# Optimization experiments

Hardware: AMD Instinct MI355X
Metric: run time of the kernel (lower is better)

Reference implementation:

```python
import jax, jax.numpy as jnp
import numpy as np

NUM_BATCHES = 8  # number of samples (unique batch ids in coords[:,0])
EPS = 1e-10


def setup_inputs() -> dict:
    key = jax.random.key(0)
    k1, k2, k3 = jax.random.split(key, 3)
    N, D, K = 65536, 64, 8192
    z_feats = jax.random.normal(k1, (N, D), dtype=jnp.float32)
    batch_ids = jnp.sort(jax.random.randint(k2, (N,), 0, NUM_BATCHES, dtype=jnp.int64))
    codebook = jax.random.normal(k3, (K, D), dtype=jnp.float32)  # embeddings.weight ~ N(0,1)
    return {"z_feats": z_feats, "batch_ids": batch_ids, "codebook": codebook}


def reference(z_feats, batch_ids, codebook):
    # --- nearest-code assignment (torch.cdist + argmin) ---
    # squared euclidean distances; argmin over sqrt(d2) == argmin over d2
    z_sq = jnp.sum(z_feats * z_feats, axis=1, keepdims=True)        # [N,1]
    c_sq = jnp.sum(codebook * codebook, axis=1)                     # [K]
    d2 = z_sq - 2.0 * (z_feats @ codebook.T) + c_sq[None, :]        # [N,K]
    encoding_indices = jnp.argmin(d2, axis=1)                       # [N] int

    # --- gather quantized features ---
    quantized_feats = codebook[encoding_indices]                    # [N,D]

    # --- losses ---
    commitment_loss = jnp.mean((z_feats - jax.lax.stop_gradient(quantized_feats)) ** 2)
    vq_loss = jnp.mean((quantized_feats - jax.lax.stop_gradient(z_feats)) ** 2)

    # --- straight-through estimator ---
    quantized_st = z_feats + jax.lax.stop_gradient(quantized_feats - z_feats)

    # --- per-sample codebook stats (vectorized over batches) ---
    K = codebook.shape[0]
    counts = jnp.zeros((NUM_BATCHES, K), jnp.float32).at[batch_ids, encoding_indices].add(1.0)
    totals = jnp.sum(counts, axis=1, keepdims=True)                 # [B,1]
    probs = counts / jnp.maximum(totals, 1.0)
    entropy = -jnp.sum(probs * jnp.log(probs + EPS), axis=1)        # [B]
    perplexity = jnp.exp(entropy)                                   # [B]
    unique_count = jnp.sum(counts > 0, axis=1).astype(jnp.float32)  # [B]
    avg_perplexity = jnp.mean(perplexity)
    avg_entropy = jnp.mean(entropy)
    avg_unique = jnp.mean(unique_count)

    return (quantized_st, vq_loss, commitment_loss, encoding_indices,
            avg_perplexity, avg_entropy, avg_unique)
```

## Files before the change

### kernel.cpp

```cpp
#include <hip/hip_runtime.h>
#include <math.h>

#define D64 64
#define NBATCH 8
#define CBAND 2.0f
#define CHUNK 128
#define NCHUNK 64
#define KSPL 2
#define CG 32
#define NGRP 256

typedef short s16x8 __attribute__((ext_vector_type(8)));
typedef float f32x4 __attribute__((ext_vector_type(4)));

#define GLOAD16(g, l) __builtin_amdgcn_global_load_lds( \
    (const __attribute__((address_space(1))) unsigned*)(g), \
    (__attribute__((address_space(3))) unsigned*)(l), 16, 0, 0)
#define GLOAD4(g, l) __builtin_amdgcn_global_load_lds( \
    (const __attribute__((address_space(1))) unsigned*)(g), \
    (__attribute__((address_space(3))) unsigned*)(l), 4, 0, 0)

__device__ inline unsigned short f2bf(float f) {
  unsigned u = __builtin_bit_cast(unsigned, f);
  unsigned r = (u + 0x7FFFu + ((u >> 16) & 1u)) >> 16;
  return (unsigned short)r;
}
__device__ inline float bflo(unsigned u) {
  return __builtin_bit_cast(float, (u & 0xFFFFu) << 16);
}
__device__ inline float bfhi(unsigned u) {
  return __builtin_bit_cast(float, u & 0xFFFF0000u);
}
__device__ inline unsigned pack32(float s) {
  unsigned u = __builtin_bit_cast(unsigned, s);
  return (u & 0x80000000u) ? ~u : (u | 0x80000000u);
}
__device__ inline float unpack32(unsigned u) {
  unsigned b = (u & 0x80000000u) ? (u ^ 0x80000000u) : ~u;
  return __builtin_bit_cast(float, b);
}

__global__ __launch_bounds__(256) void csq_cvt_kernel(
    const float* __restrict__ cb, float* __restrict__ csq,
    float* __restrict__ csqn, short* __restrict__ cbh,
    unsigned int* __restrict__ counts, unsigned* __restrict__ pminu,
    double* __restrict__ sse_parts, int K, int Npts) {
  int t = blockIdx.x * blockDim.x + threadIdx.x;
  if (t < NBATCH * K) counts[t] = 0u;
  if (t < Npts) pminu[t] = 0xFFFFFFFFu;
  if (t < 256) sse_parts[t] = 0.0;
  int row = t >> 6, lane = t & 63;
  if (row >= K) return;
  float v = cb[(size_t)row * D64 + lane];
  cbh[(size_t)row * D64 + lane] = (short)f2bf(v);
  v *= v;
  #pragma unroll
  for (int off = 32; off; off >>= 1) v += __shfl_xor(v, off, 64);
  if (lane == 0) { csq[row] = v; csqn[row] = -0.5f * v; }
}

__global__ __launch_bounds__(256, 4) void sweep_kernel(
    const float* __restrict__ z, const short* __restrict__ cbh,
    const float* __restrict__ csqn,
    unsigned short* __restrict__ bm, unsigned* __restrict__ pminu,
    int N, int K) {
  __shared__ short lcb[2][CHUNK * D64];
  __shared__ float lcsq[2][CHUNK];

  int w = threadIdx.x >> 6;
  int l = threadIdx.x & 63;
  int lr = l & 15, lg = l >> 4;
  int base = blockIdx.x * 128 + w * 32;
  int c0g = blockIdx.y * (NCHUNK / KSPL);

  s16x8 Z[2][2];
  #pragma unroll
  for (int pt = 0; pt < 2; ++pt) {
    int row = base + pt * 16 + lr;
    #pragma unroll
    for (int kh = 0; kh < 2; ++kh) {
      const float4* zp = reinterpret_cast<const float4*>(
          z + (size_t)row * D64 + kh * 32 + lg * 8);
      float4 p0 = zp[0], p1 = zp[1];
      s16x8 t;
      t[0] = (short)f2bf(p0.x); t[1] = (short)f2bf(p0.y);
      t[2] = (short)f2bf(p0.z); t[3] = (short)f2bf(p0.w);
      t[4] = (short)f2bf(p1.x); t[5] = (short)f2bf(p1.y);
      t[6] = (short)f2bf(p1.z); t[7] = (short)f2bf(p1.w);
      Z[pt][kh] = t;
    }
  }

  int sw = (lr & 7) << 4;
  int p0off = ((lr * 128 + lg * 16) ^ sw);
  int p1off = ((lr * 128 + 64 + lg * 16) ^ sw);
  int swl = (l >> 3) << 4;

  const char* cbbytes = (const char*)cbh;
#define STAGE(chunk, b)                                                       \
  {                                                                           \
    const char* src = cbbytes + (size_t)(chunk) * (CHUNK * 128);              \
    char* dstb = (char*)lcb[b];                                               \
    _Pragma("unroll")                                                         \
    for (int j = 0; j < 4; ++j) {                                             \
      int X = (w * 4 + j) * 1024 + l * 16;                                    \
      GLOAD16(src + (X ^ swl), dstb + (w * 4 + j) * 1024);                    \
    }                                                                         \
    const char* csrc = (const char*)(csqn + (chunk) * CHUNK) + (w & 1) * 256; \
    GLOAD4(csrc + l * 4, (char*)lcsq[b] + (w & 1) * 256);                     \
  }

  float gm0 = -INFINITY, gm1 = -INFINITY;

  auto do_chunk = [&](int cg, int b) {
    const char* pb0 = (const char*)lcb[b] + p0off;
    const char* pb1 = (const char*)lcb[b] + p1off;
    float g0 = -INFINITY, g1 = -INFINITY;
    #pragma unroll
    for (int i = 0; i < 8; ++i) {
      s16x8 CA0 = *(const s16x8*)(pb0 + i * 2048);
      s16x8 CA1 = *(const s16x8*)(pb1 + i * 2048);
      float4 cn = *(const float4*)(lcsq[b] + i * 16 + lg * 4);
      #pragma unroll
      for (int pt = 0; pt < 2; ++pt) {
        f32x4 acc = {cn.x, cn.y, cn.z, cn.w};
        acc = __builtin_amdgcn_mfma_f32_16x16x32_bf16(CA0, Z[pt][0], acc, 0, 0, 0);
        acc = __builtin_amdgcn_mfma_f32_16x16x32_bf16(CA1, Z[pt][1], acc, 0, 0, 0);
        float m = fmaxf(fmaxf(acc[0], acc[1]), fmaxf(acc[2], acc[3]));
        if (pt == 0) g0 = fmaxf(g0, m); else g1 = fmaxf(g1, m);
      }
    }
    #pragma unroll
    for (int pt = 0; pt < 2; ++pt) {
      float a = pt ? g1 : g0;
      float bb = __shfl_xor(a, 16, 64);
      float cc = __shfl_xor(a, 32, 64);
      float dd = __shfl_xor(a, 48, 64);
      float gmx = fmaxf(fmaxf(a, bb), fmaxf(cc, dd));
      if (pt == 0) gm0 = fmaxf(gm0, gmx); else gm1 = fmaxf(gm1, gmx);
      if (l < 16) {
        unsigned q0 = (unsigned)f2bf(-2.0f * a) |
                      ((unsigned)f2bf(-2.0f * bb) << 16);
        unsigned q1 = (unsigned)f2bf(-2.0f * cc) |
                      ((unsigned)f2bf(-2.0f * dd) << 16);
        unsigned short* rp = bm + (size_t)(base + pt * 16 + l) * NGRP + cg * 4;
        *reinterpret_cast<uint2*>(rp) = make_uint2(q0, q1);
      }
    }
  };

  STAGE(c0g, 0);
  __syncthreads();
  for (int c = 0; c < NCHUNK / KSPL; ++c) {
    if (c + 1 < NCHUNK / KSPL) STAGE(c0g + c + 1, (c + 1) & 1);
    do_chunk(c0g + c, c & 1);
    __syncthreads();
  }
  if (l < 16) {
    atomicMin(&pminu[base + l], pack32(-2.0f * gm0));
    atomicMin(&pminu[base + 16 + l], pack32(-2.0f * gm1));
  }
#undef STAGE
}

__global__ __launch_bounds__(256) void rescore_wave_kernel(
    const float* __restrict__ z, const float* __restrict__ cb,
    const float* __restrict__ csq, const unsigned short* __restrict__ bm,
    const unsigned* __restrict__ pminu, const int* __restrict__ batch_raw,
    float* __restrict__ out_idx, float* __restrict__ outq,
    unsigned int* __restrict__ counts, double* __restrict__ sse_parts,
    int N, int K) {
  int l = threadIdx.x & 63;
  int n = blockIdx.x * 4 + (threadIdx.x >> 6);

  float thr = unpack32(pminu[n]) + CBAND;
  uint2 u = reinterpret_cast<const uint2*>(bm + (size_t)n * NGRP)[l];
  float v0 = bflo(u.x), v1 = bfhi(u.x), v2 = bflo(u.y), v3 = bfhi(u.y);
  unsigned long long m0 = __ballot(v0 <= thr);
  unsigned long long m1 = __ballot(v1 <= thr);
  unsigned long long m2 = __ballot(v2 <= thr);
  unsigned long long m3 = __ballot(v3 <= thr);

  const float4* z4 = reinterpret_cast<const float4*>(z + (size_t)n * D64);
  float4 zz0 = z4[(l & 7) * 2];
  float4 zz1 = z4[(l & 7) * 2 + 1];

  auto next_group = [&]() -> int {
    if (m0) { int t = __builtin_ctzll(m0); m0 &= m0 - 1; return t * 4 + 0; }
    if (m1) { int t = __builtin_ctzll(m1); m1 &= m1 - 1; return t * 4 + 1; }
    if (m2) { int t = __builtin_ctzll(m2); m2 &= m2 - 1; return t * 4 + 2; }
    if (m3) { int t = __builtin_ctzll(m3); m3 &= m3 - 1; return t * 4 + 3; }
    return -1;
  };

  float b1 = INFINITY, b2 = INFINITY;
  int i1 = 0x7FFFFFFF, i2 = 0x7FFFFFFF;
  bool real = (l & 7) == 0;
  int code_idx = l >> 3;
  int ioff = code_idx >> 2;
  int sub = code_idx & 3;
  const float4* cbf4 = reinterpret_cast<const float4*>(cb);

  while (m0 | m1 | m2 | m3) {
    int g = next_group();
    int cbase = (g >> 2) * 128 + (g & 3) * 4;
    const float4* gb = cbf4 + (size_t)cbase * 16;
    #pragma unroll
    for (int rr = 0; rr < 4; ++rr) {
      int i = rr * 2 + ioff;
      int rel = (i * 16 + sub) * 16 + (l & 7) * 2;
      float4 q0 = gb[rel];
      float4 q1 = gb[rel + 1];
      float p = q0.x * zz0.x;
      p = fmaf(q0.y, zz0.y, p);
      p = fmaf(q0.z, zz0.z, p);
      p = fmaf(q0.w, zz0.w, p);
      p = fmaf(q1.x, zz1.x, p);
      p = fmaf(q1.y, zz1.y, p);
      p = fmaf(q1.z, zz1.z, p);
      p = fmaf(q1.w, zz1.w, p);
      p += __shfl_xor(p, 1, 64);
      p += __shfl_xor(p, 2, 64);
      p += __shfl_xor(p, 4, 64);
      int k = cbase + i * 16 + sub;
      float s = fmaf(-2.0f, p, csq[k]);
      float sv = real ? s : INFINITY;
      int kv = real ? k : 0x7FFFFFFF;
      bool bet1 = (sv < b1) || (sv == b1 && kv < i1);
      float cs = bet1 ? b1 : sv;  int ci = bet1 ? i1 : kv;
      b1 = bet1 ? sv : b1;        i1 = bet1 ? kv : i1;
      bool bet2 = (cs < b2) || (cs == b2 && ci < i2);
      b2 = bet2 ? cs : b2;        i2 = bet2 ? ci : i2;
    }
  }
  #pragma unroll
  for (int off = 1; off < 64; off <<= 1) {
    float o1 = __shfl_xor(b1, off, 64); int j1 = __shfl_xor(i1, off, 64);
    float o2 = __shfl_xor(b2, off, 64); int j2 = __shfl_xor(i2, off, 64);
    bool t1 = (o1 < b1) || (o1 == b1 && j1 < i1);
    float cs = t1 ? b1 : o1;  int ci = t1 ? i1 : j1;
    b1 = t1 ? o1 : b1;        i1 = t1 ? j1 : i1;
    bool t2 = (cs < b2) || (cs == b2 && ci < i2);
    b2 = t2 ? cs : b2;        i2 = t2 ? ci : i2;
    bool t3 = (o2 < b2) || (o2 == b2 && j2 < i2);
    b2 = t3 ? o2 : b2;        i2 = t3 ? j2 : i2;
  }

  int final_i = i1;
  if (i2 != 0x7FFFFFFF && (b2 - b1) < 1e-3f) {
    double zd = (double)z[(size_t)n * D64 + l];
    double t0 = zd - (double)cb[(size_t)i1 * D64 + l];
    double t1 = zd - (double)cb[(size_t)i2 * D64 + l];
    double d0 = t0 * t0, d1 = t1 * t1;
    #pragma unroll
    for (int off = 1; off < 64; off <<= 1) {
      d0 += __shfl_xor(d0, off, 64);
      d1 += __shfl_xor(d1, off, 64);
    }
    if (d1 < d0 || (d1 == d0 && i2 < i1)) final_i = i2;
  }

  float zl = z[(size_t)n * D64 + l];
  float ql = cb[(size_t)final_i * D64 + l];
  float tl = ql - zl;
  outq[(size_t)n * D64 + l] = zl + tl;
  double loc = (double)tl * tl;
  #pragma unroll
  for (int off = 1; off < 64; off <<= 1) loc += __shfl_xor(loc, off, 64);
  if (l == 0) {
    out_idx[n] = (float)final_i;
    int is64 = (batch_raw[N - 1] == 0) ? 1 : 0;
    int b = is64 ? batch_raw[2 * n] : batch_raw[n];
    atomicAdd(&counts[(size_t)b * K + final_i], 1u);
    atomicAdd(&sse_parts[n & 255], loc);
  }
}

__global__ __launch_bounds__(256) void stats_kernel(
    const unsigned int* __restrict__ counts,
    double* __restrict__ perp, double* __restrict__ ent,
    double* __restrict__ uniq, int K) {
  __shared__ double sh4[4], she[4], shu[4];
  int b = blockIdx.x;
  const unsigned int* c = counts + (size_t)b * K;
  int lane = threadIdx.x & 63, w = threadIdx.x >> 6;

  double tot = 0.0;
  for (int k = threadIdx.x; k < K; k += blockDim.x) tot += (double)c[k];
  #pragma unroll
  for (int off = 32; off; off >>= 1) tot += __shfl_xor(tot, off, 64);
  if (lane == 0) sh4[w] = tot;
  __syncthreads();
  double total = sh4[0] + sh4[1] + sh4[2] + sh4[3];
  double denom = fmax(total, 1.0);

  double e = 0.0, u = 0.0;
  for (int k = threadIdx.x; k < K; k += blockDim.x) {
    double cc = (double)c[k];
    double p = cc / denom;
    e -= p * log(p + 1e-10);
    if (cc > 0.0) u += 1.0;
  }
  #pragma unroll
  for (int off = 32; off; off >>= 1) {
    e += __shfl_xor(e, off, 64);
    u += __shfl_xor(u, off, 64);
  }
  if (lane == 0) { she[w] = e; shu[w] = u; }
  __syncthreads();
  if (threadIdx.x == 0) {
    double E = she[0] + she[1] + she[2] + she[3];
    double U = shu[0] + shu[1] + shu[2] + shu[3];
    ent[b] = E; perp[b] = exp(E); uniq[b] = U;
  }
}

__global__ void final_kernel(const double* __restrict__ sse_parts,
                             const double* __restrict__ perp,
                             const double* __restrict__ ent,
                             const double* __restrict__ uniq,
                             float* __restrict__ out, int N) {
  int l = threadIdx.x;
  double s = sse_parts[l] + sse_parts[l + 64] +
             sse_parts[l + 128] + sse_parts[l + 192];
  #pragma unroll
  for (int off = 1; off < 64; off <<= 1) s += __shfl_xor(s, off, 64);
  if (l == 0 && blockIdx.x == 0) {
    double mp = 0.0, me = 0.0, mu = 0.0;
    for (int b = 0; b < NBATCH; ++b) { mp += perp[b]; me += ent[b]; mu += uniq[b]; }
    mp /= NBATCH; me /= NBATCH; mu /= NBATCH;
    double loss = s / ((double)N * (double)D64);
    size_t voff = (size_t)N * D64;
    size_t coff = voff + 1;
    size_t poff = coff + 1 + (size_t)N;
    out[voff] = (float)loss;
    out[coff] = (float)loss;
    out[poff] = (float)mp;
    out[poff + 1] = (float)me;
    out[poff + 2] = (float)mu;
  }
}

extern "C" void kernel_launch(void* const* d_in, const int* in_sizes, int n_in,
                              void* d_out, int out_size, void* d_ws, size_t ws_size,
                              hipStream_t stream) {
  const float* z = (const float*)d_in[0];
  const int* bid = (const int*)d_in[1];
  const float* cb = (const float*)d_in[2];
  int N = in_sizes[1];
  int Dd = in_sizes[0] / N;
  int K = in_sizes[2] / Dd;
  float* out = (float*)d_out;

  char* ws = (char*)d_ws;
  size_t off = 0;
  auto alloc = [&](size_t bytes) {
    void* p = ws + off;
    off += (bytes + 255) & ~(size_t)255;
    return p;
  };
  unsigned int* counts = (unsigned int*)alloc((size_t)NBATCH * K * 4);
  double* sse_parts = (double*)alloc(256 * 8);
  double* perp = (double*)alloc(8 * NBATCH);
  double* ent  = (double*)alloc(8 * NBATCH);
  double* uniq = (double*)alloc(8 * NBATCH);
  float* csq = (float*)alloc((size_t)K * 4);
  float* csqn = (float*)alloc((size_t)K * 4);
  short* cbh = (short*)alloc((size_t)K * D64 * 2);
  unsigned* pminu = (unsigned*)alloc((size_t)N * 4);
  unsigned short* bm = (unsigned short*)alloc((size_t)N * NGRP * 2);

  size_t ioff = (size_t)N * Dd + 2;

  csq_cvt_kernel<<<(K * 64 + 255) / 256, 256, 0, stream>>>(
      cb, csq, csqn, cbh, counts, pminu, sse_parts, K, N);
  dim3 sg(N / 128, KSPL);
  sweep_kernel<<<sg, 256, 0, stream>>>(z, cbh, csqn, bm, pminu, N, K);
  rescore_wave_kernel<<<N / 4, 256, 0, stream>>>(
      z, cb, csq, bm, pminu, bid, out + ioff, out, counts, sse_parts, N, K);
  stats_kernel<<<NBATCH, 256, 0, stream>>>(counts, perp, ent, uniq, K);
  final_kernel<<<1, 64, 0, stream>>>(sse_parts, perp, ent, uniq, out, N);
}
```

Baseline: 189.2 us.

## Widen sweep tile to 64 rows per wave and split codebook four ways

Each wave in the sweep kernel now holds 64 query rows (four 16-row tiles) instead of 32, so every codebook fragment loaded from LDS feeds twice as many MFMAs. The codebook split grows from 2 to 4 so the grid keeps the same block count. The aim is less LDS traffic and fewer staging loads per MFMA. The cost is more registers per thread, which may reduce occupancy under the launch bound of 4, and more atomicMin calls on the per-row minimum.

```diff
diff --git a/kernel.cpp b/kernel.cpp
--- a/kernel.cpp
+++ b/kernel.cpp
@@ -6,7 +6,8 @@
 #define CBAND 2.0f
 #define CHUNK 128
 #define NCHUNK 64
-#define KSPL 2
+#define KSPL 4
+#define NCH0 (NCHUNK / KSPL)
 #define CG 32
 #define NGRP 256
 
@@ -70,12 +71,12 @@
   int w = threadIdx.x >> 6;
   int l = threadIdx.x & 63;
   int lr = l & 15, lg = l >> 4;
-  int base = blockIdx.x * 128 + w * 32;
-  int c0g = blockIdx.y * (NCHUNK / KSPL);
-
-  s16x8 Z[2][2];
-  #pragma unroll
-  for (int pt = 0; pt < 2; ++pt) {
+  int base = blockIdx.x * 256 + w * 64;
+  int c0g = blockIdx.y * NCH0;
+
+  s16x8 Z[4][2];
+  #pragma unroll
+  for (int pt = 0; pt < 4; ++pt) {
     int row = base + pt * 16 + lr;
     #pragma unroll
     for (int kh = 0; kh < 2; ++kh) {
@@ -110,38 +111,42 @@
     GLOAD4(csrc + l * 4, (char*)lcsq[b] + (w & 1) * 256);                     \
   }
 
-  float gm0 = -INFINITY, gm1 = -INFINITY;
+  float gm[4];
+  #pragma unroll
+  for (int pt = 0; pt < 4; ++pt) gm[pt] = -INFINITY;
 
   auto do_chunk = [&](int cg, int b) {
     const char* pb0 = (const char*)lcb[b] + p0off;
     const char* pb1 = (const char*)lcb[b] + p1off;
-    float g0 = -INFINITY, g1 = -INFINITY;
+    float g[4];
+    #pragma unroll
+    for (int pt = 0; pt < 4; ++pt) g[pt] = -INFINITY;
     #pragma unroll
     for (int i = 0; i < 8; ++i) {
       s16x8 CA0 = *(const s16x8*)(pb0 + i * 2048);
       s16x8 CA1 = *(const s16x8*)(pb1 + i * 2048);
       float4 cn = *(const float4*)(lcsq[b] + i * 16 + lg * 4);
       #pragma unroll
-      for (int pt = 0; pt < 2; ++pt) {
+      for (int pt = 0; pt < 4; ++pt) {
         f32x4 acc = {cn.x, cn.y, cn.z, cn.w};
         acc = __builtin_amdgcn_mfma_f32_16x16x32_bf16(CA0, Z[pt][0], acc, 0, 0, 0);
         acc = __builtin_amdgcn_mfma_f32_16x16x32_bf16(CA1, Z[pt][1], acc, 0, 0, 0);
         float m = fmaxf(fmaxf(acc[0], acc[1]), fmaxf(acc[2], acc[3]));
-        if (pt == 0) g0 = fmaxf(g0, m); else g1 = fmaxf(g1, m);
+        g[pt] = fmaxf(g[pt], m);
       }
     }
     #pragma unroll
-    for (int pt = 0; pt < 2; ++pt) {
-      float a = pt ? g1 : g0;
+    for (int pt = 0; pt < 4; ++pt) {
+      float a = g[pt];
       float bb = __shfl_xor(a, 16, 64);
-      float cc = __shfl_xor(a, 32, 64);
+      float cc2 = __shfl_xor(a, 32, 64);
       float dd = __shfl_xor(a, 48, 64);
-      float gmx = fmaxf(fmaxf(a, bb), fmaxf(cc, dd));
-      if (pt == 0) gm0 = fmaxf(gm0, gmx); else gm1 = fmaxf(gm1, gmx);
+      float gmx = fmaxf(fmaxf(a, bb), fmaxf(cc2, dd));
+      gm[pt] = fmaxf(gm[pt], gmx);
       if (l < 16) {
         unsigned q0 = (unsigned)f2bf(-2.0f * a) |
                       ((unsigned)f2bf(-2.0f * bb) << 16);
-        unsigned q1 = (unsigned)f2bf(-2.0f * cc) |
+        unsigned q1 = (unsigned)f2bf(-2.0f * cc2) |
                       ((unsigned)f2bf(-2.0f * dd) << 16);
         unsigned short* rp = bm + (size_t)(base + pt * 16 + l) * NGRP + cg * 4;
         *reinterpret_cast<uint2*>(rp) = make_uint2(q0, q1);
@@ -151,14 +156,15 @@
 
   STAGE(c0g, 0);
   __syncthreads();
-  for (int c = 0; c < NCHUNK / KSPL; ++c) {
-    if (c + 1 < NCHUNK / KSPL) STAGE(c0g + c + 1, (c + 1) & 1);
+  for (int c = 0; c < NCH0; ++c) {
+    if (c + 1 < NCH0) STAGE(c0g + c + 1, (c + 1) & 1);
     do_chunk(c0g + c, c & 1);
     __syncthreads();
   }
   if (l < 16) {
-    atomicMin(&pminu[base + l], pack32(-2.0f * gm0));
-    atomicMin(&pminu[base + 16 + l], pack32(-2.0f * gm1));
+    #pragma unroll
+    for (int pt = 0; pt < 4; ++pt)
+      atomicMin(&pminu[base + pt * 16 + l], pack32(-2.0f * gm[pt]));
   }
 #undef STAGE
 }
@@ -374,7 +380,7 @@
 
   csq_cvt_kernel<<<(K * 64 + 255) / 256, 256, 0, stream>>>(
       cb, csq, csqn, cbh, counts, pminu, sse_parts, K, N);
-  dim3 sg(N / 128, KSPL);
+  dim3 sg(N / 256, KSPL);
   sweep_kernel<<<sg, 256, 0, stream>>>(z, cbh, csqn, bm, pminu, N, K);
   rescore_wave_kernel<<<N / 4, 256, 0, stream>>>(
       z, cb, csq, bm, pminu, bid, out + ioff, out, counts, sse_parts, N, K);
```

After: 398.8 us. 111% more time.
